# Kernel optimization log

Hardware: AMD Instinct MI355X
Metric: run time of the kernel (lower is better)

## Reference

```python
import jax, jax.numpy as jnp
import numpy as np

N_NODES = 100000
N_EDGES = 1600000
C = 256            # in_channels == out_channels
NUM_BUNDLES = 64
BUNDLE_DIM = 2
NUM_GRAPHS = 128
BN_EPS = 1e-5


def setup_inputs() -> dict:
    key = jax.random.key(0)
    ks = jax.random.split(key, 12)
    x = jax.random.normal(ks[0], (N_NODES, C), dtype=jnp.float32)
    edge_index = jax.random.randint(ks[1], (2, N_EDGES), 0, N_NODES, dtype=jnp.int64)
    batch = jnp.sort(jax.random.randint(ks[2], (N_NODES,), 0, NUM_GRAPHS, dtype=jnp.int64))
    s = 0.05
    # struct_enc MLP: Linear(C, 2*NB) -> GELU -> Linear(2*NB, NB)
    se_w1 = jax.random.normal(ks[3], (C, 2 * NUM_BUNDLES), dtype=jnp.float32) * s
    se_b1 = jnp.zeros((2 * NUM_BUNDLES,), dtype=jnp.float32)
    se_w2 = jax.random.normal(ks[4], (2 * NUM_BUNDLES, NUM_BUNDLES), dtype=jnp.float32) * s
    se_b2 = jnp.zeros((NUM_BUNDLES,), dtype=jnp.float32)
    # LimConv.lin: Linear(C, C)
    lin_w = jax.random.normal(ks[5], (C, C), dtype=jnp.float32) * s
    lin_b = jnp.zeros((C,), dtype=jnp.float32)
    # BatchNorm1d affine params
    bn_gamma = jnp.ones((C,), dtype=jnp.float32)
    bn_beta = jnp.zeros((C,), dtype=jnp.float32)
    return {"x": x, "edge_index": edge_index, "batch": batch,
            "se_w1": se_w1, "se_b1": se_b1, "se_w2": se_w2, "se_b2": se_b2,
            "lin_w": lin_w, "lin_b": lin_b, "bn_gamma": bn_gamma, "bn_beta": bn_beta}


def _lim_layer(x, batch, se_w1, se_b1, se_w2, se_b2, lin_w, lin_b, bn_gamma, bn_beta):
    n = x.shape[0]
    # vector field: [N, NB, 2, fiber]
    vf = x.reshape(n, NUM_BUNDLES, BUNDLE_DIM, -1)
    # struct_enc MLP -> per-bundle angle (tanh-squashed), euler map to SO(2)
    h1 = jax.nn.gelu(x @ se_w1 + se_b1, approximate=False)
    ang = jnp.tanh(h1 @ se_w2 + se_b2)          # [N, NB]
    c, s = jnp.cos(ang), jnp.sin(ang)
    # R[n,b] = [[c,-s],[s,c]]  -> [N, NB, 2, 2]
    rot = jnp.stack([jnp.stack([c, -s], axis=-1),
                     jnp.stack([s, c], axis=-1)], axis=-2)
    # rotate fibers
    vf = jnp.einsum('nbij,nbjf->nbif', rot, vf)
    h = vf.reshape(n, C) @ lin_w + lin_b
    # global mean pool over graphs, then broadcast back to nodes
    sums = jax.ops.segment_sum(h, batch, num_segments=NUM_GRAPHS)
    cnts = jax.ops.segment_sum(jnp.ones((n,), h.dtype), batch, num_segments=NUM_GRAPHS)
    hmean = sums / jnp.maximum(cnts, 1.0)[:, None]
    h = hmean[batch]
    # inverse rotation (R^T)
    vf = h.reshape(n, NUM_BUNDLES, BUNDLE_DIM, -1)
    vf = jnp.einsum('nbji,nbjf->nbif', rot, vf)
    h = vf.reshape(n, C)
    # residual (dim_in == dim_out)
    h = x + h
    # dropout p=0 / eval -> identity. BatchNorm1d with batch statistics.
    mu = jnp.mean(h, axis=0)
    var = jnp.var(h, axis=0)
    h = (h - mu) * jax.lax.rsqrt(var + BN_EPS) * bn_gamma + bn_beta
    return h


def reference(x, edge_index, batch, se_w1, se_b1, se_w2, se_b2, lin_w, lin_b, bn_gamma, bn_beta):
    # edge_index is unused when num_gnn == 0 (struct_enc is an MLP), as in the source.
    del edge_index
    return _lim_layer(x, batch, se_w1, se_b1, se_w2, se_b2, lin_w, lin_b, bn_gamma, bn_beta)
```

## Files before the change

kernel.cpp:

```cpp
#include <hip/hip_runtime.h>
#include <hip/hip_bf16.h>
#include <math.h>

#define N_NODES 100000
#define C 256
#define NB 64
#define H1D 128
#define NG 128
#define BN_EPS 1e-5f

#define BLKN 32
#define ROWS 128
#define SUBT 4
#define NBLK1 ((N_NODES + ROWS - 1) / ROWS)
#define NPART NBLK1

#define GREC 769

#define OFF_GSUMS 0
#define OFF_BNSUM (NG * GREC)
#define OFF_BNSQ  (OFF_BNSUM + 256)
#define ZERO_FLOATS (OFF_BNSQ + 256)
#define OFF_HMEAN ZERO_FLOATS
#define OFF_WT1   (OFF_HMEAN + NG * C)
#define OFF_WT2   (OFF_WT1 + 16896)
#define OFF_CSN   (OFF_WT2 + 4352)
#define OFF_PBN   (OFF_CSN + N_NODES * 64)

#define WT1_LD 264
#define WT2_LD 136
#define XS_LD  272

typedef __attribute__((ext_vector_type(8))) short bf16x8;
typedef __attribute__((ext_vector_type(4))) float f32x4;

struct __align__(8) bf4 { __hip_bfloat16 x, y, z, w; };

__device__ __forceinline__ float bf2f(__hip_bfloat16 h) { return __bfloat162float(h); }

__device__ __forceinline__ float fast_tanh(float y) {
    float e = __expf(2.f * y);
    return 1.f - 2.f / (e + 1.f);
}
__device__ __forceinline__ float fast_gelu(float v) {
    float u = 0.7978845608f * (v + 0.044715f * v * v * v);
    return 0.5f * v * (1.f + fast_tanh(u));
}

__global__ __launch_bounds__(256)
void k0_prep(const float* __restrict__ W1, const float* __restrict__ W2,
             __hip_bfloat16* __restrict__ Wt1, __hip_bfloat16* __restrict__ Wt2)
{
    const int t0 = threadIdx.x + blockIdx.x * 256;
    const int stride = gridDim.x * 256;
    for (int i = t0; i < 128 * 256; i += stride) {
        int n = i >> 8, k = i & 255;
        Wt1[n * WT1_LD + k] = __float2bfloat16(W1[k * 128 + n]);
    }
    for (int i = t0; i < 64 * 128; i += stride) {
        int n = i >> 7, k = i & 127;
        Wt2[n * WT2_LD + k] = __float2bfloat16(W2[k * 64 + n]);
    }
}

__global__ __launch_bounds__(256, 6)
void k1_angles_rot_pool(const float* __restrict__ x,
                        const int* __restrict__ batch,
                        const __hip_bfloat16* __restrict__ Wt1g,
                        const float* __restrict__ b1,
                        const __hip_bfloat16* __restrict__ Wt2g,
                        const float* __restrict__ b2,
                        float* __restrict__ gsums,
                        float* __restrict__ pbn,
                        __hip_bfloat16* __restrict__ csng)
{
    __shared__ __hip_bfloat16 xs[BLKN][XS_LD];
    __shared__ char sm_u[BLKN * WT2_LD * 2];
    __shared__ int gsh[BLKN];
    auto h1s = (__hip_bfloat16 (*)[WT2_LD])sm_u;
    auto csn = (__hip_bfloat16 (*)[132])sm_u;

    const int t = threadIdx.x;
    const int w = t >> 6;
    const int l = t & 63;
    const int lo = l & 15, quad = l >> 4;

    const short* w1base = (const short*)Wt1g + (w * 32 + lo) * WT1_LD + quad * 8;
    const int mw = w >> 1;
    const int nb0 = (w & 1) * 32;
    const short* w2base = (const short*)Wt2g + (nb0 + lo) * WT2_LD + quad * 8;
    const float bb1_0 = b1[w * 32 + lo];
    const float bb1_1 = b1[w * 32 + 16 + lo];
    const float bb2_0 = b2[nb0 + lo];
    const float bb2_1 = b2[nb0 + 16 + lo];

    const int c = t;
    const int b = c >> 2;
    const int idx2 = c & 3;
    float xc_a = 0.f, xs_a = 0.f, st = 0.f, rcnt = 0.f;
    float xm = 0.f, xq = 0.f;
    int gprev = -1;

#define FLUSH_G(gidx) do {                               \
        float* rec = gsums + (size_t)(gidx) * GREC;      \
        atomicAdd(&rec[c], xc_a);                        \
        atomicAdd(&rec[256 + c], xs_a);                  \
        atomicAdd(&rec[512 + c], st);                    \
        if (c == 0) atomicAdd(&rec[768], rcnt);          \
    } while (0)

    for (int sub = 0; sub < SUBT; ++sub) {
        const int n0 = blockIdx.x * ROWS + sub * BLKN;
        if (n0 >= N_NODES) break;

        #pragma unroll
        for (int m = 0; m < 8; ++m) {
            int idx = t + m * 256;
            int r = idx >> 6, c4 = (idx & 63) * 4;
            float4 v = *(const float4*)(x + (size_t)(n0 + r) * C + c4);
            bf4 pk;
            pk.x = __float2bfloat16(v.x); pk.y = __float2bfloat16(v.y);
            pk.z = __float2bfloat16(v.z); pk.w = __float2bfloat16(v.w);
            *(bf4*)&xs[r][c4] = pk;
        }
        if (t < BLKN) gsh[t] = batch[n0 + t];
        __syncthreads();

        f32x4 acc1[2][2];
        #pragma unroll
        for (int mt = 0; mt < 2; ++mt) { acc1[mt][0] = (f32x4)0.f; acc1[mt][1] = (f32x4)0.f; }
        #pragma unroll
        for (int k = 0; k < 8; ++k) {
            bf16x8 bA = *(const bf16x8*)(w1base + k * 32);
            bf16x8 bB = *(const bf16x8*)(w1base + 16 * WT1_LD + k * 32);
            #pragma unroll
            for (int mt = 0; mt < 2; ++mt) {
                bf16x8 afr = *(const bf16x8*)&xs[mt * 16 + lo][k * 32 + quad * 8];
                acc1[mt][0] = __builtin_amdgcn_mfma_f32_16x16x32_bf16(afr, bA, acc1[mt][0], 0, 0, 0);
                acc1[mt][1] = __builtin_amdgcn_mfma_f32_16x16x32_bf16(afr, bB, acc1[mt][1], 0, 0, 0);
            }
        }
        #pragma unroll
        for (int nt = 0; nt < 2; ++nt) {
            const float bb = nt ? bb1_1 : bb1_0;
            #pragma unroll
            for (int mt = 0; mt < 2; ++mt) {
                #pragma unroll
                for (int r = 0; r < 4; ++r) {
                    float v = fast_gelu(acc1[mt][nt][r] + bb);
                    h1s[mt * 16 + quad * 4 + r][w * 32 + nt * 16 + lo] = __float2bfloat16(v);
                }
            }
        }
        __syncthreads();

        f32x4 acc2[2];
        acc2[0] = (f32x4)0.f; acc2[1] = (f32x4)0.f;
        #pragma unroll
        for (int k = 0; k < 4; ++k) {
            bf16x8 afr = *(const bf16x8*)&h1s[mw * 16 + lo][k * 32 + quad * 8];
            bf16x8 bA = *(const bf16x8*)(w2base + k * 32);
            bf16x8 bB = *(const bf16x8*)(w2base + 16 * WT2_LD + k * 32);
            acc2[0] = __builtin_amdgcn_mfma_f32_16x16x32_bf16(afr, bA, acc2[0], 0, 0, 0);
            acc2[1] = __builtin_amdgcn_mfma_f32_16x16x32_bf16(afr, bB, acc2[1], 0, 0, 0);
        }
        __syncthreads();

        #pragma unroll
        for (int nt = 0; nt < 2; ++nt) {
            const int col = nb0 + nt * 16 + lo;
            const float bb = nt ? bb2_1 : bb2_0;
            #pragma unroll
            for (int r = 0; r < 4; ++r) {
                float a = fast_tanh(acc2[nt][r] + bb);
                union { unsigned int u; __hip_bfloat16 h[2]; } p;
                p.h[0] = __float2bfloat16(__cosf(a));
                p.h[1] = __float2bfloat16(__sinf(a));
                *(unsigned int*)&csn[mw * 16 + quad * 4 + r][2 * col] = p.u;
            }
        }
        __syncthreads();

        #pragma unroll
        for (int m = 0; m < 4; ++m) {
            int idx = t + m * 256;
            int row = idx >> 5;
            int q = (idx & 31);
            uint2 v = *(const uint2*)&csn[row][q * 4];
            *(uint2*)(csng + (size_t)(n0 + row) * 128 + q * 4) = v;
        }

        #pragma unroll 8
        for (int r = 0; r < BLKN; ++r) {
            const int g = gsh[r];
            if (g != gprev) {
                if (gprev >= 0) FLUSH_G(gprev);
                xc_a = 0.f; xs_a = 0.f; st = 0.f; rcnt = 0.f;
                gprev = g;
            }
            const float xv = bf2f(xs[r][c]);
            union { unsigned int u; __hip_bfloat16 h[2]; } cs;
            cs.u = *(const unsigned int*)&csn[r][2 * b];
            const float cv = bf2f(cs.h[0]);
            const float sv = bf2f(cs.h[1]);
            xc_a += xv * cv;
            xs_a += xv * sv;
            xm += xv;
            xq += xv * xv;
            st += (idx2 == 0) ? cv : (idx2 == 1) ? sv : (idx2 == 2) ? cv * cv : cv * sv;
            rcnt += 1.f;
        }
        __syncthreads();
    }

    if (gprev >= 0) FLUSH_G(gprev);
    pbn[(size_t)blockIdx.x * 512 + t] = xm;
    pbn[(size_t)blockIdx.x * 512 + 256 + t] = xq;
#undef FLUSH_G
}

__global__ __launch_bounds__(256)
void k2_hmean_stats(const float* __restrict__ gsums,
                    const float* __restrict__ pbn,
                    const float* __restrict__ lin_w, const float* __restrict__ lin_b,
                    float* __restrict__ hmean,
                    float* __restrict__ bnsum, float* __restrict__ bnsq)
{
    __shared__ float xc[C], xsv[C], bs4[C], grot[C], hm[C];
    __shared__ float cnt_sh;
    const int g = blockIdx.x;
    const int t = threadIdx.x;

    {
        const int ch = 4 * g + (t >> 6);
        const int lane = t & 63;
        float acc = 0.f;
        for (int r = lane; r < NPART; r += 64)
            acc += pbn[(size_t)r * 512 + ch];
        #pragma unroll
        for (int off = 32; off; off >>= 1) acc += __shfl_down(acc, off);
        if (lane == 0) {
            if (ch < 256) atomicAdd(&bnsum[ch], acc);
            else          atomicAdd(&bnsq[ch - 256], acc);
        }
    }

    const float* rec = gsums + (size_t)g * GREC;
    xc[t]  = rec[t];
    xsv[t] = rec[256 + t];
    bs4[t] = rec[512 + t];
    if (t == 0) cnt_sh = rec[768];
    __syncthreads();

    const int b = t >> 2, idx2 = t & 3, i2 = idx2 >> 1;
    grot[t] = (i2 == 0) ? (xc[t] - xsv[t + 2]) : (xsv[t - 2] + xc[t]);
    __syncthreads();

    float a0 = 0.f, a1 = 0.f, a2 = 0.f, a3 = 0.f;
    #pragma unroll 4
    for (int k = 0; k < C; k += 4) {
        a0 += grot[k + 0] * lin_w[(size_t)(k + 0) * C + t];
        a1 += grot[k + 1] * lin_w[(size_t)(k + 1) * C + t];
        a2 += grot[k + 2] * lin_w[(size_t)(k + 2) * C + t];
        a3 += grot[k + 3] * lin_w[(size_t)(k + 3) * C + t];
    }
    const float cnt = cnt_sh;
    const float hv = (cnt > 0.f) ? ((a0 + a1 + a2 + a3) / cnt + lin_b[t]) : 0.f;
    hm[t] = hv;
    hmean[g * C + t] = hv;
    __syncthreads();

    if (cnt > 0.f) {
        const int f = idx2 & 1;
        const float h0 = hm[4 * b + f];
        const float h1 = hm[4 * b + 2 + f];
        const float CV = bs4[4 * b + 0], SV = bs4[4 * b + 1];
        const float CC = bs4[4 * b + 2], CS = bs4[4 * b + 3];
        const float SS = cnt - CC;
        float sumc, sqc;
        if (i2 == 0) {
            sumc = h0 * CV + h1 * SV;
            sqc  = 2.f * (h0 * xc[t] + h1 * xsv[t])
                 + h0 * h0 * CC + 2.f * h0 * h1 * CS + h1 * h1 * SS;
        } else {
            sumc = -h0 * SV + h1 * CV;
            sqc  = 2.f * (-h0 * xsv[t] + h1 * xc[t])
                 + h0 * h0 * SS - 2.f * h0 * h1 * CS + h1 * h1 * CC;
        }
        atomicAdd(&bnsum[t], sumc);
        atomicAdd(&bnsq[t], sqc);
    }
}

__global__ __launch_bounds__(256, 4)
void k4_fused(const float* __restrict__ x,
              const int* __restrict__ batch,
              const __hip_bfloat16* __restrict__ csng,
              const float* __restrict__ hmean,
              const float* __restrict__ bnsum, const float* __restrict__ bnsq,
              const float* __restrict__ gamma, const float* __restrict__ beta,
              float* __restrict__ out)
{
    __shared__ float mul_s[C], add_s[C];
    const int t = threadIdx.x;
    {
        const float inv_n = 1.0f / (float)N_NODES;
        const float mu = bnsum[t] * inv_n;
        const float var = bnsq[t] * inv_n - mu * mu;
        const float inv = rsqrtf(var + BN_EPS);
        const float m = gamma[t] * inv;
        mul_s[t] = m;
        add_s[t] = beta[t] - mu * m;
    }
    __syncthreads();
    const int s = t >> 6;
    const int cg = t & 63;
    const float4 mm = *(const float4*)&mul_s[cg * 4];
    const float4 aa = *(const float4*)&add_s[cg * 4];

    for (int base = blockIdx.x * 4; base < N_NODES; base += gridDim.x * 4) {
        const int n = base + s;
        if (n < N_NODES) {
            const int g = batch[n];
            const float4 hm = *(const float4*)(hmean + (size_t)g * C + cg * 4);
            union { unsigned int u; __hip_bfloat16 h[2]; } cs;
            cs.u = *(const unsigned int*)(csng + (size_t)n * 128 + cg * 2);
            const float cv = bf2f(cs.h[0]);
            const float sv = bf2f(cs.h[1]);
            const float4 xv = *(const float4*)(x + (size_t)n * C + cg * 4);
            float4 o;
            o.x = (xv.x + cv * hm.x + sv * hm.z) * mm.x + aa.x;
            o.y = (xv.y + cv * hm.y + sv * hm.w) * mm.y + aa.y;
            o.z = (xv.z - sv * hm.x + cv * hm.z) * mm.z + aa.z;
            o.w = (xv.w - sv * hm.y + cv * hm.w) * mm.w + aa.w;
            *(float4*)(out + (size_t)n * C + cg * 4) = o;
        }
    }
}

extern "C" void kernel_launch(void* const* d_in, const int* in_sizes, int n_in,
                              void* d_out, int out_size, void* d_ws, size_t ws_size,
                              hipStream_t stream)
{
    const float* x      = (const float*)d_in[0];
    const int* batch    = (const int*)d_in[2];
    const float* W1     = (const float*)d_in[3];
    const float* b1     = (const float*)d_in[4];
    const float* W2     = (const float*)d_in[5];
    const float* b2     = (const float*)d_in[6];
    const float* lin_w  = (const float*)d_in[7];
    const float* lin_b  = (const float*)d_in[8];
    const float* gamma  = (const float*)d_in[9];
    const float* beta   = (const float*)d_in[10];

    float* ws    = (float*)d_ws;
    float* gsums = ws + OFF_GSUMS;
    float* bnsum = ws + OFF_BNSUM;
    float* bnsq  = ws + OFF_BNSQ;
    float* hmean = ws + OFF_HMEAN;
    __hip_bfloat16* Wt1  = (__hip_bfloat16*)(ws + OFF_WT1);
    __hip_bfloat16* Wt2  = (__hip_bfloat16*)(ws + OFF_WT2);
    __hip_bfloat16* csng = (__hip_bfloat16*)(ws + OFF_CSN);
    float* pbn   = ws + OFF_PBN;
    float* out   = (float*)d_out;

    hipMemsetAsync(gsums, 0, ZERO_FLOATS * sizeof(float), stream);

    k0_prep<<<32, 256, 0, stream>>>(W1, W2, Wt1, Wt2);
    k1_angles_rot_pool<<<NBLK1, 256, 0, stream>>>(x, batch, Wt1, b1, Wt2, b2,
                                                  gsums, pbn, csng);
    k2_hmean_stats<<<NG, 256, 0, stream>>>(gsums, pbn, lin_w, lin_b, hmean, bnsum, bnsq);
    k4_fused<<<2048, 256, 0, stream>>>(x, batch, csng, hmean, bnsum, bnsq,
                                       gamma, beta, out);
}
```

Before: 320.7 us.

## Prefetch next x tile into registers, shrink rows per block, coalesce partial reduction

The first kernel now loads the next 32-row x tile and its batch ids into registers while the current tile is being processed, so global load latency overlaps with the MFMA work. Rows per block are halved, which doubles the grid and the number of partial BN records. The second kernel now has each block reduce a contiguous chunk of partial rows across all 512 channels with coalesced loads, replacing the strided per-channel gather. The register prefetch raises VGPR pressure, and the larger grid adds more atomics on the per-graph sums.

```diff
diff --git a/kernel.cpp b/kernel.cpp
--- a/kernel.cpp
+++ b/kernel.cpp
@@ -10,8 +10,8 @@
 #define BN_EPS 1e-5f
 
 #define BLKN 32
-#define ROWS 128
-#define SUBT 4
+#define ROWS 64
+#define SUBT 2
 #define NBLK1 ((N_NODES + ROWS - 1) / ROWS)
 #define NPART NBLK1
 
@@ -94,6 +94,9 @@
     const float bb2_0 = b2[nb0 + lo];
     const float bb2_1 = b2[nb0 + 16 + lo];
 
+    const int pr = t >> 6;
+    const int pc4 = (t & 63) * 4;
+
     const int c = t;
     const int b = c >> 2;
     const int idx2 = c & 3;
@@ -109,21 +112,37 @@
         if (c == 0) atomicAdd(&rec[768], rcnt);          \
     } while (0)
 
+    float4 pf[8];
+    int pb = 0;
+    {
+        const int n0 = blockIdx.x * ROWS;
+        #pragma unroll
+        for (int m = 0; m < 8; ++m)
+            pf[m] = *(const float4*)(x + (size_t)(n0 + pr + m * 4) * C + pc4);
+        if (t < BLKN) pb = batch[n0 + t];
+    }
+
     for (int sub = 0; sub < SUBT; ++sub) {
         const int n0 = blockIdx.x * ROWS + sub * BLKN;
         if (n0 >= N_NODES) break;
 
         #pragma unroll
         for (int m = 0; m < 8; ++m) {
-            int idx = t + m * 256;
-            int r = idx >> 6, c4 = (idx & 63) * 4;
-            float4 v = *(const float4*)(x + (size_t)(n0 + r) * C + c4);
             bf4 pk;
-            pk.x = __float2bfloat16(v.x); pk.y = __float2bfloat16(v.y);
-            pk.z = __float2bfloat16(v.z); pk.w = __float2bfloat16(v.w);
-            *(bf4*)&xs[r][c4] = pk;
-        }
-        if (t < BLKN) gsh[t] = batch[n0 + t];
+            pk.x = __float2bfloat16(pf[m].x); pk.y = __float2bfloat16(pf[m].y);
+            pk.z = __float2bfloat16(pf[m].z); pk.w = __float2bfloat16(pf[m].w);
+            *(bf4*)&xs[pr + m * 4][pc4] = pk;
+        }
+        if (t < BLKN) gsh[t] = pb;
+
+        const int n1 = n0 + BLKN;
+        const bool more = (sub + 1 < SUBT) && (n1 < N_NODES);
+        if (more) {
+            #pragma unroll
+            for (int m = 0; m < 8; ++m)
+                pf[m] = *(const float4*)(x + (size_t)(n1 + pr + m * 4) * C + pc4);
+            if (t < BLKN) pb = batch[n1 + t];
+        }
         __syncthreads();
 
         f32x4 acc1[2][2];
@@ -232,16 +251,17 @@
     const int t = threadIdx.x;
 
     {
-        const int ch = 4 * g + (t >> 6);
-        const int lane = t & 63;
-        float acc = 0.f;
-        for (int r = lane; r < NPART; r += 64)
-            acc += pbn[(size_t)r * 512 + ch];
-        #pragma unroll
-        for (int off = 32; off; off >>= 1) acc += __shfl_down(acc, off);
-        if (lane == 0) {
-            if (ch < 256) atomicAdd(&bnsum[ch], acc);
-            else          atomicAdd(&bnsq[ch - 256], acc);
+        const int chunk = (NPART + NG - 1) / NG;
+        const int r0 = g * chunk;
+        const int r1 = (r0 + chunk < NPART) ? (r0 + chunk) : NPART;
+        if (r0 < r1) {
+            float a0 = 0.f, a1 = 0.f;
+            for (int r = r0; r < r1; ++r) {
+                a0 += pbn[(size_t)r * 512 + t];
+                a1 += pbn[(size_t)r * 512 + 256 + t];
+            }
+            atomicAdd(&bnsum[t], a0);
+            atomicAdd(&bnsq[t], a1);
         }
     }
 
```

Result: faster. 297.4 us (-7.3%).
